# Performance work log

Measured on AMD Instinct MI355X. Metric: run time of the kernel, lower is better.

## Reference

```python
import jax, jax.numpy as jnp
import numpy as np

HEADS = 10
DIM_HEAD = 64
C = 640
N_TOK = 1024          # (1024//32)**2 tokens per image
IMG_NUMS = 3          # total_length = id_length + 1
ID_LENGTH = 2
SA = 0.5
NEG_INF = -1e9


def _build_story_mask(key):
    # Faithful to cal_attn_mask_xl: one random row of columns shared by all
    # images, columns beyond the id_length reference images zeroed, and each
    # image's own block forced True; then broadcast over query tokens.
    L = IMG_NUMS * N_TOK
    base = jax.random.uniform(key, (1, L)) < SA                  # [1, L]
    bm = jnp.tile(base, (IMG_NUMS, 1))                           # [img, L]
    col = jnp.arange(L)
    bm = jnp.where(col[None, :] >= ID_LENGTH * N_TOK, False, bm)
    self_block = (col // N_TOK)[None, :] == jnp.arange(IMG_NUMS)[:, None]
    bm = bm | self_block                                         # [img, L]
    return jnp.repeat(bm, N_TOK, axis=0)                         # [L, L]


def setup_inputs() -> dict:
    key = jax.random.key(0)
    ks = jax.random.split(key, 7)
    B_total = 2 * IMG_NUMS
    hidden_states = jax.random.normal(ks[0], (B_total, N_TOK, C), dtype=jnp.float32)
    mask = _build_story_mask(ks[1])
    s = 1.0 / np.sqrt(C)
    Wq = jax.random.normal(ks[2], (C, HEADS * DIM_HEAD), dtype=jnp.float32) * s
    Wk = jax.random.normal(ks[3], (C, HEADS * DIM_HEAD), dtype=jnp.float32) * s
    Wv = jax.random.normal(ks[4], (C, HEADS * DIM_HEAD), dtype=jnp.float32) * s
    Wout = jax.random.normal(ks[5], (HEADS * DIM_HEAD, C), dtype=jnp.float32) * s
    bout = jnp.zeros((C,), dtype=jnp.float32)
    return {"hidden_states": hidden_states, "mask": mask,
            "Wq": Wq, "Wk": Wk, "Wv": Wv, "Wout": Wout, "bout": bout}


def reference(hidden_states, mask, Wq, Wk, Wv, Wout, bout):
    # __call1__ with encoder_hidden_states=None: fuse img_nums images into one
    # long sequence per CFG branch, then masked SDPA.
    B_total, n_tok, c = hidden_states.shape
    img_nums = B_total // 2
    L = img_nums * n_tok
    x = hidden_states.reshape(2, L, c)                       # [2, L, C]

    q = jnp.einsum('bsc,cd->bsd', x, Wq).reshape(2, L, HEADS, DIM_HEAD)
    k = jnp.einsum('bsc,cd->bsd', x, Wk).reshape(2, L, HEADS, DIM_HEAD)
    v = jnp.einsum('bsc,cd->bsd', x, Wv).reshape(2, L, HEADS, DIM_HEAD)

    scale = 1.0 / jnp.sqrt(jnp.asarray(DIM_HEAD, dtype=q.dtype))
    scores = jnp.einsum('bqhd,bkhd->bhqk', q, k) * scale     # [2, H, L, L]
    scores = jnp.where(mask[None, None, :, :], scores, NEG_INF)
    attn = jax.nn.softmax(scores, axis=-1)
    out = jnp.einsum('bhqk,bkhd->bqhd', attn, v)             # [2, L, H, Dh]
    out = out.reshape(B_total, n_tok, HEADS * DIM_HEAD)
    return jnp.einsum('bsd,dc->bsc', out, Wout) + bout
```

## Files before the change

### kernel.cpp

```cpp
#include <hip/hip_runtime.h>
#include <cstdint>
#include <cstddef>

typedef _Float16 f16;
typedef _Float16 f16x8 __attribute__((ext_vector_type(8)));
typedef _Float16 f16x4 __attribute__((ext_vector_type(4)));
typedef float f32x4 __attribute__((ext_vector_type(4)));

#define MFMA32(a, b, c) __builtin_amdgcn_mfma_f32_16x16x32_f16((a), (b), (c), 0, 0, 0)
#define MFMA16(a, b, c) __builtin_amdgcn_mfma_f32_16x16x16f16((a), (b), (c), 0, 0, 0)

#define EXP2F(x) exp2f(x)
#define LOG2E 1.44269504088896340736f

__device__ __forceinline__ void gl_lds16(const f16* g, f16* l) {
    __builtin_amdgcn_global_load_lds((const __attribute__((address_space(1))) void*)g,
                                     (__attribute__((address_space(3))) void*)l, 16, 0, 0);
}

__global__ __launch_bounds__(256) void k_cvt_x(const float4* __restrict__ x, f16x4* __restrict__ xb) {
    const int i = blockIdx.x * 256 + threadIdx.x;
    const float4 v = x[i];
    f16x4 o;
    o[0] = (f16)v.x; o[1] = (f16)v.y; o[2] = (f16)v.z; o[3] = (f16)v.w;
    xb[i] = o;
}

__global__ __launch_bounds__(256) void k_cvt_w(const float* __restrict__ Wq, const float* __restrict__ Wk,
                                               const float* __restrict__ Wv, const float* __restrict__ Wo,
                                               f16* __restrict__ WT, f16* __restrict__ WoT) {
    __shared__ float tile[32][33];
    const int z = blockIdx.z;
    const float* src = (z == 0) ? Wq : (z == 1) ? Wk : (z == 2) ? Wv : Wo;
    f16* dst = (z < 3) ? (WT + (size_t)z * 640 * 640) : WoT;
    const float scale = (z == 0) ? 0.125f * LOG2E : 1.0f;
    const int k0 = blockIdx.x * 32, n0 = blockIdx.y * 32;
    const int t = threadIdx.x;
#pragma unroll
    for (int i = 0; i < 4; i++) {
        const int idx = i * 256 + t;
        const int r = idx >> 5, c = idx & 31;
        tile[r][c] = src[(size_t)(k0 + r) * 640 + n0 + c];
    }
    __syncthreads();
#pragma unroll
    for (int i = 0; i < 4; i++) {
        const int idx = i * 256 + t;
        const int r = idx >> 5, c = idx & 31;
        dst[(size_t)(n0 + r) * 640 + k0 + c] = (f16)(tile[c][r] * scale);
    }
}

__global__ __launch_bounds__(256) void k_gemm(const f16* __restrict__ A, const f16* __restrict__ B,
                                              f16* __restrict__ qb, f16* __restrict__ kb, f16* __restrict__ vtb,
                                              float* __restrict__ out, const float* __restrict__ bias,
                                              const int mode) {
    __shared__ f16 As[128 * 40];
    __shared__ f16 Bs[128 * 40];
    const int t = threadIdx.x;
    const int wave = t >> 6, lane = t & 63, quad = lane >> 4, l16 = lane & 15;
    const int wm = wave >> 1, wn = wave & 1;
    const long m0 = (long)blockIdx.x * 128, n0 = (long)blockIdx.y * 128;
    const int srow = t >> 2, skc = t & 3;

    const f32x4 zero = {0.f, 0.f, 0.f, 0.f};
    f32x4 acc[4][4];
#pragma unroll
    for (int i = 0; i < 4; i++)
#pragma unroll
        for (int j = 0; j < 4; j++) acc[i][j] = zero;

    const f16* gA1 = A + (m0 + srow) * 640 + skc * 8;
    const f16* gA2 = A + (m0 + 64 + srow) * 640 + skc * 8;
    const f16* gB1 = B + (n0 + srow) * 640 + skc * 8;
    const f16* gB2 = B + (n0 + 64 + srow) * 640 + skc * 8;
    f16* sA1 = As + srow * 40 + skc * 8;
    f16* sA2 = As + (64 + srow) * 40 + skc * 8;
    f16* sB1 = Bs + srow * 40 + skc * 8;
    f16* sB2 = Bs + (64 + srow) * 40 + skc * 8;

    for (int kt = 0; kt < 20; kt++) {
        const int ko = kt * 32;
        const f16x8 a1 = *(const f16x8*)(gA1 + ko);
        const f16x8 a2 = *(const f16x8*)(gA2 + ko);
        const f16x8 b1 = *(const f16x8*)(gB1 + ko);
        const f16x8 b2 = *(const f16x8*)(gB2 + ko);
        __syncthreads();
        *(f16x8*)sA1 = a1;
        *(f16x8*)sA2 = a2;
        *(f16x8*)sB1 = b1;
        *(f16x8*)sB2 = b2;
        __syncthreads();
        f16x8 af[4], bfr[4];
#pragma unroll
        for (int mi = 0; mi < 4; mi++) af[mi] = *(const f16x8*)(As + (wm * 64 + mi * 16 + l16) * 40 + quad * 8);
#pragma unroll
        for (int ni = 0; ni < 4; ni++) bfr[ni] = *(const f16x8*)(Bs + (wn * 64 + ni * 16 + l16) * 40 + quad * 8);
#pragma unroll
        for (int mi = 0; mi < 4; mi++)
#pragma unroll
            for (int ni = 0; ni < 4; ni++) acc[mi][ni] = MFMA32(af[mi], bfr[ni], acc[mi][ni]);
    }

    if (mode == 0) {
        const int b = (int)(m0 / 3072);
        const int which = (int)(n0 / 640);
        const int hd0 = (int)(n0 - (long)which * 640);
        if (which < 2) {
            f16* dst = (which == 0) ? qb : kb;
#pragma unroll
            for (int ni = 0; ni < 4; ni++) {
                const int hd = hd0 + wn * 64 + ni * 16 + l16;
                const int h = hd >> 6, d = hd & 63;
#pragma unroll
                for (int mi = 0; mi < 4; mi++) {
                    const long l0 = m0 - (long)b * 3072 + wm * 64 + mi * 16 + quad * 4;
                    f16* p = dst + ((long)(b * 10 + h) * 3072 + l0) * 64 + d;
#pragma unroll
                    for (int j = 0; j < 4; j++) p[(long)j * 64] = (f16)acc[mi][ni][j];
                }
            }
        } else {
#pragma unroll
            for (int ni = 0; ni < 4; ni++) {
                const int hd = hd0 + wn * 64 + ni * 16 + l16;
                const int h = hd >> 6, d = hd & 63;
#pragma unroll
                for (int mi = 0; mi < 4; mi++) {
                    const long l0 = m0 - (long)b * 3072 + wm * 64 + mi * 16 + quad * 4;
                    f16x4 tmp;
#pragma unroll
                    for (int j = 0; j < 4; j++) tmp[j] = (f16)acc[mi][ni][j];
                    *(f16x4*)(vtb + ((size_t)(b * 10 + h) * 64 + d) * 3072 + l0) = tmp;
                }
            }
        }
    } else {
#pragma unroll
        for (int ni = 0; ni < 4; ni++) {
            const long gc = n0 + wn * 64 + ni * 16 + l16;
            const float bs = bias[gc];
#pragma unroll
            for (int mi = 0; mi < 4; mi++) {
                const long r0 = m0 + wm * 64 + mi * 16 + quad * 4;
                float* p = out + r0 * 640 + gc;
#pragma unroll
                for (int j = 0; j < 4; j++) p[(long)j * 640] = acc[mi][ni][j] + bs;
            }
        }
    }
}

__global__ __launch_bounds__(256, 3) void k_attn(const f16* __restrict__ q, const f16* __restrict__ k,
                                                 const f16* __restrict__ vT, const unsigned char* __restrict__ mask,
                                                 f16* __restrict__ ao) {
    __shared__ __align__(16) unsigned char smem[40960];

    const int t = threadIdx.x;
    const int w = t >> 6, lane = t & 63, quad = lane >> 4, l16 = lane & 15;
    const int bh = blockIdx.y, b = bh / 10, h = bh - b * 10;
    const int qt = (blockIdx.x < 16) ? (32 + (int)blockIdx.x) : ((int)blockIdx.x - 16);
    const int q0 = qt * 64;
    const int img = q0 >> 10;
    const int kmax = (img == 2) ? 3072 : 2048;
    const int nIter = kmax >> 6;
    float* bias_s = (float*)(smem + 32768);

    int mmode;
    if (mask[1] && mask[2] && mask[3]) mmode = 0;
    else if (mask[7] == 0x3f) mmode = 2;
    else mmode = 1;
    const int msz = (mmode == 0) ? 1 : 4;
    const int mhi = (mmode == 2) ? 3 : 0;
    const unsigned char* mrow = mask + (size_t)img * 1024 * 3072 * msz;

    for (int i = t; i < 2048; i += 256)
        bias_s[i] = (mrow[(size_t)i * msz + mhi] != 0) ? 0.f : -1e9f;

    const int r8 = lane >> 3, cch = lane & 7;
    const f16* kg = k + (size_t)bh * 3072 * 64;
    const f16* vg = vT + (size_t)bh * 64 * 3072;
    const int wrow0 = w * 16;

    {
        f16* K0 = (f16*)smem;
        f16* V0 = (f16*)(smem + 16384);
#pragma unroll
        for (int i = 0; i < 2; i++) {
            const int row = wrow0 + i * 8 + r8;
            gl_lds16(kg + (size_t)row * 64 + ((cch ^ (row & 7)) * 8), K0 + (wrow0 + i * 8) * 64);
            gl_lds16(vg + (size_t)row * 3072 + ((cch ^ (row & 7)) * 8), V0 + (wrow0 + i * 8) * 64);
        }
    }

    f16x8 qf0, qf1;
    {
        const f16* qp = q + ((size_t)bh * 3072 + q0 + w * 16 + l16) * 64 + quad * 8;
        qf0 = *(const f16x8*)qp;
        qf1 = *(const f16x8*)(qp + 32);
    }

    const f32x4 zero = {0.f, 0.f, 0.f, 0.f};
    f32x4 O[4];
#pragma unroll
    for (int i = 0; i < 4; i++) O[i] = zero;
    float m_i = -1e30f, l_i = 0.f;

    for (int it = 0; it < nIter; it++) {
        __syncthreads();
        const f16* Kc = (const f16*)(smem + (it & 1) * 8192);
        const f16* Vc = (const f16*)(smem + 16384 + (it & 1) * 8192);
        if (it + 1 < nIter) {
            const int k0n = (it + 1) << 6;
            f16* Kn = (f16*)(smem + ((it + 1) & 1) * 8192);
            f16* Vn = (f16*)(smem + 16384 + ((it + 1) & 1) * 8192);
#pragma unroll
            for (int i = 0; i < 2; i++) {
                const int row = wrow0 + i * 8 + r8;
                gl_lds16(kg + (size_t)(k0n + row) * 64 + ((cch ^ (row & 7)) * 8), Kn + (wrow0 + i * 8) * 64);
                gl_lds16(vg + (size_t)row * 3072 + k0n + ((cch ^ (row & 7)) * 8), Vn + (wrow0 + i * 8) * 64);
            }
        }

        f32x4 s[4];
#pragma unroll
        for (int kt = 0; kt < 4; kt++) {
            const int krow = kt * 16 + l16;
            const int ksw = krow & 7;
            const f16* kr = Kc + krow * 64;
            const f16x8 kf0 = *(const f16x8*)(kr + ((quad ^ ksw) * 8));
            const f16x8 kf1 = *(const f16x8*)(kr + (((4 + quad) ^ ksw) * 8));
            s[kt] = MFMA32(kf0, qf0, zero);
            s[kt] = MFMA32(kf1, qf1, s[kt]);
        }
        if (it * 64 < 2048) {
#pragma unroll
            for (int kt = 0; kt < 4; kt++)
                s[kt] += *(const f32x4*)(bias_s + it * 64 + kt * 16 + quad * 4);
        }

        float tmax = -1e30f;
#pragma unroll
        for (int kt = 0; kt < 4; kt++)
#pragma unroll
            for (int j = 0; j < 4; j++) tmax = fmaxf(tmax, s[kt][j]);
        tmax = fmaxf(tmax, __shfl_xor(tmax, 16));
        tmax = fmaxf(tmax, __shfl_xor(tmax, 32));
        const float mn = fmaxf(m_i, tmax);
        const float al = EXP2F(m_i - mn);
        m_i = mn;
        f16x4 pk[4];
        float rs = 0.f;
#pragma unroll
        for (int kt = 0; kt < 4; kt++) {
#pragma unroll
            for (int j = 0; j < 4; j++) {
                const float pv = EXP2F(s[kt][j] - mn);
                rs += pv;
                pk[kt][j] = (f16)pv;
            }
        }
        rs += __shfl_xor(rs, 16);
        rs += __shfl_xor(rs, 32);
        l_i = l_i * al + rs;

#pragma unroll
        for (int mtd = 0; mtd < 4; mtd++) O[mtd] *= al;
#pragma unroll
        for (int kt = 0; kt < 4; kt++) {
#pragma unroll
            for (int mtd = 0; mtd < 4; mtd++) {
                const int rv = mtd * 16 + l16;
                const int ch = 2 * kt + (quad >> 1);
                const f16x4 vf = *(const f16x4*)(Vc + rv * 64 + ((ch ^ (rv & 7)) * 8) + (quad & 1) * 4);
                O[mtd] = MFMA16(vf, pk[kt], O[mtd]);
            }
        }
    }

    const float inv = 1.0f / l_i;
    f16* orow = ao + ((size_t)(b * 3072 + q0 + w * 16 + l16)) * 640 + h * 64;
#pragma unroll
    for (int mtd = 0; mtd < 4; mtd++) {
        f16x4 o;
#pragma unroll
        for (int j = 0; j < 4; j++) o[j] = (f16)(O[mtd][j] * inv);
        *(f16x4*)(orow + mtd * 16 + quad * 4) = o;
    }
}

extern "C" void kernel_launch(void* const* d_in, const int* in_sizes, int n_in,
                              void* d_out, int out_size, void* d_ws, size_t ws_size,
                              hipStream_t stream) {
    (void)in_sizes; (void)n_in; (void)out_size; (void)ws_size;
    const float* x = (const float*)d_in[0];
    const unsigned char* mask = (const unsigned char*)d_in[1];
    const float* Wq = (const float*)d_in[2];
    const float* Wk = (const float*)d_in[3];
    const float* Wv = (const float*)d_in[4];
    const float* Wo = (const float*)d_in[5];
    const float* bout = (const float*)d_in[6];
    float* out = (float*)d_out;

    f16* xb  = (f16*)d_ws;
    f16* WT  = xb + 6144 * 640;
    f16* WoT = WT + 1920 * 640;
    f16* qb  = WoT + 640 * 640;
    f16* kb  = qb + 20 * 3072 * 64;
    f16* vtb = kb + 20 * 3072 * 64;

    k_cvt_x<<<3840, 256, 0, stream>>>((const float4*)x, (f16x4*)xb);
    k_cvt_w<<<dim3(20, 20, 4), 256, 0, stream>>>(Wq, Wk, Wv, Wo, WT, WoT);
    k_gemm<<<dim3(48, 15), 256, 0, stream>>>(xb, WT, qb, kb, vtb, nullptr, nullptr, 0);
    k_attn<<<dim3(48, 20), 256, 0, stream>>>(qb, kb, vtb, mask, xb );
    k_gemm<<<dim3(48, 5), 256, 0, stream>>>(xb, WoT, nullptr, nullptr, nullptr, out, bout, 1);
}
```

Baseline: 250.7 us.

## Process two query tiles per wave in attention, permute V layout, split out-projection GEMM

The attention kernel now uses 128-thread blocks where each wave handles 32 query rows as two 16-row tiles. Each K and V fragment read from LDS is reused for both tiles, halving shared-memory reads per MFMA. The V projection store permutes columns within 64-token chunks so the PV step can load 8-wide vectors instead of 4-wide, and the exp uses the hardware exp2 builtin. The output projection moves to a dedicated 64x128-tile GEMM with twice as many blocks, which raises register pressure in attention but lowers LDS traffic.

Result: faster. 228.7 us (-8.8%).

```diff
diff --git a/kernel.cpp b/kernel.cpp
--- a/kernel.cpp
+++ b/kernel.cpp
@@ -10,8 +10,18 @@
 #define MFMA32(a, b, c) __builtin_amdgcn_mfma_f32_16x16x32_f16((a), (b), (c), 0, 0, 0)
 #define MFMA16(a, b, c) __builtin_amdgcn_mfma_f32_16x16x16f16((a), (b), (c), 0, 0, 0)
 
+#if __has_builtin(__builtin_amdgcn_exp2f)
+#define EXP2F(x) __builtin_amdgcn_exp2f(x)
+#else
 #define EXP2F(x) exp2f(x)
+#endif
+
 #define LOG2E 1.44269504088896340736f
+
+__device__ __forceinline__ f16x4 pack4(float a, float b, float c, float d) {
+    f16x4 r; r[0] = (f16)a; r[1] = (f16)b; r[2] = (f16)c; r[3] = (f16)d;
+    return r;
+}
 
 __device__ __forceinline__ void gl_lds16(const f16* g, f16* l) {
     __builtin_amdgcn_global_load_lds((const __attribute__((address_space(1))) void*)g,
@@ -52,9 +62,7 @@
 }
 
 __global__ __launch_bounds__(256) void k_gemm(const f16* __restrict__ A, const f16* __restrict__ B,
-                                              f16* __restrict__ qb, f16* __restrict__ kb, f16* __restrict__ vtb,
-                                              float* __restrict__ out, const float* __restrict__ bias,
-                                              const int mode) {
+                                              f16* __restrict__ qb, f16* __restrict__ kb, f16* __restrict__ vtb) {
     __shared__ f16 As[128 * 40];
     __shared__ f16 Bs[128 * 40];
     const int t = threadIdx.x;
@@ -102,56 +110,101 @@
             for (int ni = 0; ni < 4; ni++) acc[mi][ni] = MFMA32(af[mi], bfr[ni], acc[mi][ni]);
     }
 
-    if (mode == 0) {
-        const int b = (int)(m0 / 3072);
-        const int which = (int)(n0 / 640);
-        const int hd0 = (int)(n0 - (long)which * 640);
-        if (which < 2) {
-            f16* dst = (which == 0) ? qb : kb;
-#pragma unroll
-            for (int ni = 0; ni < 4; ni++) {
-                const int hd = hd0 + wn * 64 + ni * 16 + l16;
-                const int h = hd >> 6, d = hd & 63;
-#pragma unroll
-                for (int mi = 0; mi < 4; mi++) {
-                    const long l0 = m0 - (long)b * 3072 + wm * 64 + mi * 16 + quad * 4;
-                    f16* p = dst + ((long)(b * 10 + h) * 3072 + l0) * 64 + d;
-#pragma unroll
-                    for (int j = 0; j < 4; j++) p[(long)j * 64] = (f16)acc[mi][ni][j];
-                }
+    const int b = (int)(m0 / 3072);
+    const int which = (int)(n0 / 640);
+    const int hd0 = (int)(n0 - (long)which * 640);
+    if (which < 2) {
+        f16* dst = (which == 0) ? qb : kb;
+#pragma unroll
+        for (int ni = 0; ni < 4; ni++) {
+            const int hd = hd0 + wn * 64 + ni * 16 + l16;
+            const int h = hd >> 6, d = hd & 63;
+#pragma unroll
+            for (int mi = 0; mi < 4; mi++) {
+                const long l0 = m0 - (long)b * 3072 + wm * 64 + mi * 16 + quad * 4;
+                f16* p = dst + ((long)(b * 10 + h) * 3072 + l0) * 64 + d;
+#pragma unroll
+                for (int j = 0; j < 4; j++) p[(long)j * 64] = (f16)acc[mi][ni][j];
             }
-        } else {
-#pragma unroll
-            for (int ni = 0; ni < 4; ni++) {
-                const int hd = hd0 + wn * 64 + ni * 16 + l16;
-                const int h = hd >> 6, d = hd & 63;
-#pragma unroll
-                for (int mi = 0; mi < 4; mi++) {
-                    const long l0 = m0 - (long)b * 3072 + wm * 64 + mi * 16 + quad * 4;
-                    f16x4 tmp;
-#pragma unroll
-                    for (int j = 0; j < 4; j++) tmp[j] = (f16)acc[mi][ni][j];
-                    *(f16x4*)(vtb + ((size_t)(b * 10 + h) * 64 + d) * 3072 + l0) = tmp;
-                }
+        }
+    } else {
+#pragma unroll
+        for (int ni = 0; ni < 4; ni++) {
+            const int hd = hd0 + wn * 64 + ni * 16 + l16;
+            const int h = hd >> 6, d = hd & 63;
+#pragma unroll
+            for (int mi = 0; mi < 4; mi++) {
+                const long l0 = m0 - (long)b * 3072 + wm * 64 + mi * 16 + quad * 4;
+                const long col = (l0 & ~63L) + quad * 16 + mi * 4;
+                f16x4 tmp;
+#pragma unroll
+                for (int j = 0; j < 4; j++) tmp[j] = (f16)acc[mi][ni][j];
+                *(f16x4*)(vtb + ((size_t)(b * 10 + h) * 64 + d) * 3072 + col) = tmp;
             }
         }
-    } else {
-#pragma unroll
-        for (int ni = 0; ni < 4; ni++) {
-            const long gc = n0 + wn * 64 + ni * 16 + l16;
-            const float bs = bias[gc];
-#pragma unroll
-            for (int mi = 0; mi < 4; mi++) {
-                const long r0 = m0 + wm * 64 + mi * 16 + quad * 4;
-                float* p = out + r0 * 640 + gc;
-#pragma unroll
-                for (int j = 0; j < 4; j++) p[(long)j * 640] = acc[mi][ni][j] + bs;
-            }
-        }
-    }
-}
-
-__global__ __launch_bounds__(256, 3) void k_attn(const f16* __restrict__ q, const f16* __restrict__ k,
+    }
+}
+
+__global__ __launch_bounds__(256) void k_gemmo(const f16* __restrict__ A, const f16* __restrict__ B,
+                                               float* __restrict__ out, const float* __restrict__ bias) {
+    __shared__ f16 As[64 * 40];
+    __shared__ f16 Bs[128 * 40];
+    const int t = threadIdx.x;
+    const int wave = t >> 6, lane = t & 63, quad = lane >> 4, l16 = lane & 15;
+    const int wm = wave >> 1, wn = wave & 1;
+    const long m0 = (long)blockIdx.x * 64, n0 = (long)blockIdx.y * 128;
+    const int srow = t >> 2, skc = t & 3;
+
+    const f32x4 zero = {0.f, 0.f, 0.f, 0.f};
+    f32x4 acc[2][4];
+#pragma unroll
+    for (int i = 0; i < 2; i++)
+#pragma unroll
+        for (int j = 0; j < 4; j++) acc[i][j] = zero;
+
+    const f16* gA = A + (m0 + srow) * 640 + skc * 8;
+    const f16* gB1 = B + (n0 + srow) * 640 + skc * 8;
+    const f16* gB2 = B + (n0 + 64 + srow) * 640 + skc * 8;
+    f16* sA = As + srow * 40 + skc * 8;
+    f16* sB1 = Bs + srow * 40 + skc * 8;
+    f16* sB2 = Bs + (64 + srow) * 40 + skc * 8;
+
+    for (int kt = 0; kt < 20; kt++) {
+        const int ko = kt * 32;
+        const f16x8 a1 = *(const f16x8*)(gA + ko);
+        const f16x8 b1 = *(const f16x8*)(gB1 + ko);
+        const f16x8 b2 = *(const f16x8*)(gB2 + ko);
+        __syncthreads();
+        *(f16x8*)sA = a1;
+        *(f16x8*)sB1 = b1;
+        *(f16x8*)sB2 = b2;
+        __syncthreads();
+        f16x8 af[2], bfr[4];
+#pragma unroll
+        for (int mi = 0; mi < 2; mi++) af[mi] = *(const f16x8*)(As + (wm * 32 + mi * 16 + l16) * 40 + quad * 8);
+#pragma unroll
+        for (int ni = 0; ni < 4; ni++) bfr[ni] = *(const f16x8*)(Bs + (wn * 64 + ni * 16 + l16) * 40 + quad * 8);
+#pragma unroll
+        for (int mi = 0; mi < 2; mi++)
+#pragma unroll
+            for (int ni = 0; ni < 4; ni++) acc[mi][ni] = MFMA32(af[mi], bfr[ni], acc[mi][ni]);
+    }
+
+#pragma unroll
+    for (int ni = 0; ni < 4; ni++) {
+        const long gc = n0 + wn * 64 + ni * 16 + l16;
+        const float bs = bias[gc];
+#pragma unroll
+        for (int mi = 0; mi < 2; mi++) {
+            const long r0 = m0 + wm * 32 + mi * 16 + quad * 4;
+            float* p = out + r0 * 640 + gc;
+#pragma unroll
+            for (int j = 0; j < 4; j++) p[(long)j * 640] = acc[mi][ni][j] + bs;
+        }
+    }
+}
+
+__global__ __launch_bounds__(128, 2) void k_attn(const f16* __restrict__ q, const f16* __restrict__ k,
                                                  const f16* __restrict__ vT, const unsigned char* __restrict__ mask,
                                                  f16* __restrict__ ao) {
     __shared__ __align__(16) unsigned char smem[40960];
@@ -174,118 +227,150 @@
     const int mhi = (mmode == 2) ? 3 : 0;
     const unsigned char* mrow = mask + (size_t)img * 1024 * 3072 * msz;
 
-    for (int i = t; i < 2048; i += 256)
+    for (int i = t; i < 2048; i += 128)
         bias_s[i] = (mrow[(size_t)i * msz + mhi] != 0) ? 0.f : -1e9f;
 
     const int r8 = lane >> 3, cch = lane & 7;
     const f16* kg = k + (size_t)bh * 3072 * 64;
     const f16* vg = vT + (size_t)bh * 64 * 3072;
-    const int wrow0 = w * 16;
+    const int wrow0 = w * 32;
 
     {
         f16* K0 = (f16*)smem;
         f16* V0 = (f16*)(smem + 16384);
 #pragma unroll
-        for (int i = 0; i < 2; i++) {
+        for (int i = 0; i < 4; i++) {
             const int row = wrow0 + i * 8 + r8;
             gl_lds16(kg + (size_t)row * 64 + ((cch ^ (row & 7)) * 8), K0 + (wrow0 + i * 8) * 64);
             gl_lds16(vg + (size_t)row * 3072 + ((cch ^ (row & 7)) * 8), V0 + (wrow0 + i * 8) * 64);
         }
     }
 
-    f16x8 qf0, qf1;
+    f16x8 qfA0, qfA1, qfB0, qfB1;
     {
-        const f16* qp = q + ((size_t)bh * 3072 + q0 + w * 16 + l16) * 64 + quad * 8;
-        qf0 = *(const f16x8*)qp;
-        qf1 = *(const f16x8*)(qp + 32);
-    }
+        const f16* qp = q + ((size_t)bh * 3072 + q0 + w * 32 + l16) * 64 + quad * 8;
+        qfA0 = *(const f16x8*)qp;
+        qfA1 = *(const f16x8*)(qp + 32);
+        qfB0 = *(const f16x8*)(qp + 16 * 64);
+        qfB1 = *(const f16x8*)(qp + 16 * 64 + 32);
+    }
+
+    const int s7 = l16 & 7;
+    const int bK0 = l16 * 128 + ((quad ^ s7) * 16);
+    const int bK1 = l16 * 128 + (((quad + 4) ^ s7) * 16);
+    const int bV0 = l16 * 128 + (((2 * quad) ^ s7) * 16);
+    const int bV1 = l16 * 128 + (((2 * quad + 1) ^ s7) * 16);
 
     const f32x4 zero = {0.f, 0.f, 0.f, 0.f};
-    f32x4 O[4];
-#pragma unroll
-    for (int i = 0; i < 4; i++) O[i] = zero;
-    float m_i = -1e30f, l_i = 0.f;
+    f32x4 OA[4], OB[4];
+#pragma unroll
+    for (int i = 0; i < 4; i++) { OA[i] = zero; OB[i] = zero; }
+    float mA = -1e30f, lA = 0.f, mB = -1e30f, lB = 0.f;
 
     for (int it = 0; it < nIter; it++) {
         __syncthreads();
-        const f16* Kc = (const f16*)(smem + (it & 1) * 8192);
-        const f16* Vc = (const f16*)(smem + 16384 + (it & 1) * 8192);
+        const char* Kb = (const char*)smem + (it & 1) * 8192;
+        const char* Vb = (const char*)smem + 16384 + (it & 1) * 8192;
         if (it + 1 < nIter) {
             const int k0n = (it + 1) << 6;
             f16* Kn = (f16*)(smem + ((it + 1) & 1) * 8192);
             f16* Vn = (f16*)(smem + 16384 + ((it + 1) & 1) * 8192);
 #pragma unroll
-            for (int i = 0; i < 2; i++) {
+            for (int i = 0; i < 4; i++) {
                 const int row = wrow0 + i * 8 + r8;
                 gl_lds16(kg + (size_t)(k0n + row) * 64 + ((cch ^ (row & 7)) * 8), Kn + (wrow0 + i * 8) * 64);
                 gl_lds16(vg + (size_t)row * 3072 + k0n + ((cch ^ (row & 7)) * 8), Vn + (wrow0 + i * 8) * 64);
             }
         }
 
-        f32x4 s[4];
+        f32x4 sA[4], sB[4];
 #pragma unroll
         for (int kt = 0; kt < 4; kt++) {
-            const int krow = kt * 16 + l16;
-            const int ksw = krow & 7;
-            const f16* kr = Kc + krow * 64;
-            const f16x8 kf0 = *(const f16x8*)(kr + ((quad ^ ksw) * 8));
-            const f16x8 kf1 = *(const f16x8*)(kr + (((4 + quad) ^ ksw) * 8));
-            s[kt] = MFMA32(kf0, qf0, zero);
-            s[kt] = MFMA32(kf1, qf1, s[kt]);
+            const f16x8 kf0 = *(const f16x8*)(Kb + bK0 + kt * 2048);
+            const f16x8 kf1 = *(const f16x8*)(Kb + bK1 + kt * 2048);
+            sA[kt] = MFMA32(kf0, qfA0, zero);
+            sA[kt] = MFMA32(kf1, qfA1, sA[kt]);
+            sB[kt] = MFMA32(kf0, qfB0, zero);
+            sB[kt] = MFMA32(kf1, qfB1, sB[kt]);
         }
         if (it * 64 < 2048) {
 #pragma unroll
-            for (int kt = 0; kt < 4; kt++)
-                s[kt] += *(const f32x4*)(bias_s + it * 64 + kt * 16 + quad * 4);
-        }
-
-        float tmax = -1e30f;
+            for (int kt = 0; kt < 4; kt++) {
+                const f32x4 bv = *(const f32x4*)(bias_s + it * 64 + kt * 16 + quad * 4);
+                sA[kt] += bv;
+                sB[kt] += bv;
+            }
+        }
+
+        float tmaxA = sA[0][0], tmaxB = sB[0][0];
 #pragma unroll
         for (int kt = 0; kt < 4; kt++)
 #pragma unroll
-            for (int j = 0; j < 4; j++) tmax = fmaxf(tmax, s[kt][j]);
-        tmax = fmaxf(tmax, __shfl_xor(tmax, 16));
-        tmax = fmaxf(tmax, __shfl_xor(tmax, 32));
-        const float mn = fmaxf(m_i, tmax);
-        const float al = EXP2F(m_i - mn);
-        m_i = mn;
-        f16x4 pk[4];
-        float rs = 0.f;
+            for (int j = 0; j < 4; j++) {
+                tmaxA = fmaxf(tmaxA, sA[kt][j]);
+                tmaxB = fmaxf(tmaxB, sB[kt][j]);
+            }
+        tmaxA = fmaxf(tmaxA, __shfl_xor(tmaxA, 16));
+        tmaxA = fmaxf(tmaxA, __shfl_xor(tmaxA, 32));
+        tmaxB = fmaxf(tmaxB, __shfl_xor(tmaxB, 16));
+        tmaxB = fmaxf(tmaxB, __shfl_xor(tmaxB, 32));
+        const float mnA = fmaxf(mA, tmaxA);
+        const float mnB = fmaxf(mB, tmaxB);
+        const float alA = EXP2F(mA - mnA);
+        const float alB = EXP2F(mB - mnB);
+        mA = mnA; mB = mnB;
+        f16x4 pkA[4], pkB[4];
+        float rsA = 0.f, rsB = 0.f;
 #pragma unroll
         for (int kt = 0; kt < 4; kt++) {
-#pragma unroll
-            for (int j = 0; j < 4; j++) {
-                const float pv = EXP2F(s[kt][j] - mn);
-                rs += pv;
-                pk[kt][j] = (f16)pv;
-            }
-        }
-        rs += __shfl_xor(rs, 16);
-        rs += __shfl_xor(rs, 32);
-        l_i = l_i * al + rs;
-
-#pragma unroll
-        for (int mtd = 0; mtd < 4; mtd++) O[mtd] *= al;
-#pragma unroll
-        for (int kt = 0; kt < 4; kt++) {
-#pragma unroll
-            for (int mtd = 0; mtd < 4; mtd++) {
-                const int rv = mtd * 16 + l16;
-                const int ch = 2 * kt + (quad >> 1);
-                const f16x4 vf = *(const f16x4*)(Vc + rv * 64 + ((ch ^ (rv & 7)) * 8) + (quad & 1) * 4);
-                O[mtd] = MFMA16(vf, pk[kt], O[mtd]);
-            }
-        }
-    }
-
-    const float inv = 1.0f / l_i;
-    f16* orow = ao + ((size_t)(b * 3072 + q0 + w * 16 + l16)) * 640 + h * 64;
+            const float a0 = EXP2F(sA[kt][0] - mnA), a1 = EXP2F(sA[kt][1] - mnA);
+            const float a2 = EXP2F(sA[kt][2] - mnA), a3 = EXP2F(sA[kt][3] - mnA);
+            rsA += (a0 + a1) + (a2 + a3);
+            pkA[kt] = pack4(a0, a1, a2, a3);
+            const float b0 = EXP2F(sB[kt][0] - mnB), b1 = EXP2F(sB[kt][1] - mnB);
+            const float b2 = EXP2F(sB[kt][2] - mnB), b3 = EXP2F(sB[kt][3] - mnB);
+            rsB += (b0 + b1) + (b2 + b3);
+            pkB[kt] = pack4(b0, b1, b2, b3);
+        }
+        rsA += __shfl_xor(rsA, 16);
+        rsA += __shfl_xor(rsA, 32);
+        rsB += __shfl_xor(rsB, 16);
+        rsB += __shfl_xor(rsB, 32);
+        lA = lA * alA + rsA;
+        lB = lB * alB + rsB;
+
+#pragma unroll
+        for (int mtd = 0; mtd < 4; mtd++) { OA[mtd] *= alA; OB[mtd] *= alB; }
+#pragma unroll
+        for (int mtd = 0; mtd < 4; mtd++) {
+            const f16x8 v80 = *(const f16x8*)(Vb + bV0 + mtd * 2048);
+            const f16x8 v81 = *(const f16x8*)(Vb + bV1 + mtd * 2048);
+            const f16x4 vf0 = __builtin_shufflevector(v80, v80, 0, 1, 2, 3);
+            const f16x4 vf1 = __builtin_shufflevector(v80, v80, 4, 5, 6, 7);
+            const f16x4 vf2 = __builtin_shufflevector(v81, v81, 0, 1, 2, 3);
+            const f16x4 vf3 = __builtin_shufflevector(v81, v81, 4, 5, 6, 7);
+            OA[mtd] = MFMA16(vf0, pkA[0], OA[mtd]);
+            OA[mtd] = MFMA16(vf1, pkA[1], OA[mtd]);
+            OA[mtd] = MFMA16(vf2, pkA[2], OA[mtd]);
+            OA[mtd] = MFMA16(vf3, pkA[3], OA[mtd]);
+            OB[mtd] = MFMA16(vf0, pkB[0], OB[mtd]);
+            OB[mtd] = MFMA16(vf1, pkB[1], OB[mtd]);
+            OB[mtd] = MFMA16(vf2, pkB[2], OB[mtd]);
+            OB[mtd] = MFMA16(vf3, pkB[3], OB[mtd]);
+        }
+    }
+
+    const float invA = 1.0f / lA;
+    const float invB = 1.0f / lB;
+    f16* orowA = ao + ((size_t)(b * 3072 + q0 + w * 32 + l16)) * 640 + h * 64;
+    f16* orowB = orowA + (size_t)16 * 640;
 #pragma unroll
     for (int mtd = 0; mtd < 4; mtd++) {
-        f16x4 o;
-#pragma unroll
-        for (int j = 0; j < 4; j++) o[j] = (f16)(O[mtd][j] * inv);
-        *(f16x4*)(orow + mtd * 16 + quad * 4) = o;
+        f16x4 oa, ob;
+#pragma unroll
+        for (int j = 0; j < 4; j++) { oa[j] = (f16)(OA[mtd][j] * invA); ob[j] = (f16)(OB[mtd][j] * invB); }
+        *(f16x4*)(orowA + mtd * 16 + quad * 4) = oa;
+        *(f16x4*)(orowB + mtd * 16 + quad * 4) = ob;
     }
 }
 
@@ -311,7 +396,7 @@
 
     k_cvt_x<<<3840, 256, 0, stream>>>((const float4*)x, (f16x4*)xb);
     k_cvt_w<<<dim3(20, 20, 4), 256, 0, stream>>>(Wq, Wk, Wv, Wo, WT, WoT);
-    k_gemm<<<dim3(48, 15), 256, 0, stream>>>(xb, WT, qb, kb, vtb, nullptr, nullptr, 0);
-    k_attn<<<dim3(48, 20), 256, 0, stream>>>(qb, kb, vtb, mask, xb );
-    k_gemm<<<dim3(48, 5), 256, 0, stream>>>(xb, WoT, nullptr, nullptr, nullptr, out, bout, 1);
-}
+    k_gemm<<<dim3(48, 15), 256, 0, stream>>>(xb, WT, qb, kb, vtb);
+    k_attn<<<dim3(48, 20), 128, 0, stream>>>(qb, kb, vtb, mask, xb );
+    k_gemmo<<<dim3(96, 5), 256, 0, stream>>>(xb, WoT, out, bout);
+}
```
